# Kernel tuning notes

Measured on AMD Instinct MI355X. Metric: run time of the kernel, lower is better.

## Reference

```python
import jax, jax.numpy as jnp
import numpy as np
from jax import lax

N = 2_097_152  # grid length
WENO5_MULT_BIAS = 0.1


def _conv1d(x, w, b, pad):
    # x: [1, C_in, L], w: [C_out, C_in, K] -> [1, C_out, L]
    y = lax.conv_general_dilated(x, w, window_strides=(1,), padding=[(pad, pad)],
                                 dimension_numbers=('NCH', 'OIH', 'NCH'))
    return y + b[None, :, None]


def _inner_nn_weno5(dif, w1, b1, w2, b2, w3, b3, w4, b4, w5, b5, w6, b6):
    # dif: [N] -> multiplier signal [N] in (0,1) via sigmoid
    x = dif[None, None, :]
    x = jax.nn.elu(_conv1d(x, w1, b1, 2))
    x = jax.nn.elu(_conv1d(x, w2, b2, 2))
    x = jax.nn.elu(_conv1d(x, w3, b3, 0))
    x = jax.nn.elu(_conv1d(x, w4, b4, 0))
    x = jax.nn.elu(_conv1d(x, w5, b5, 1))
    x = jax.nn.sigmoid(_conv1d(x, w6, b6, 0))
    return x[0, 0, :]


def _avg_diff(uu):
    # centered average of forward differences, replicated at the edges -> [N]
    dif = uu[1:] - uu[:-1]
    dif_left = jnp.concatenate([dif, dif[-1:]])
    dif_right = jnp.concatenate([dif[:1], dif])
    return 0.5 * dif_left + 0.5 * dif_right


def _fluxes_minus(u):
    f0 = (11 * u[3:-2] - 7 * u[4:-1] + 2 * u[5:]) / 6
    f1 = (2 * u[2:-3] + 5 * u[3:-2] - u[4:-1]) / 6
    f2 = (-u[1:-4] + 5 * u[2:-3] + 2 * u[3:-2]) / 6
    return f0, f1, f2


def _betas_minus(u):
    b0 = 13 / 12 * (u[3:-2] - 2 * u[4:-1] + u[5:]) ** 2 + 1 / 4 * (3 * u[3:-2] - 4 * u[4:-1] + u[5:]) ** 2
    b1 = 13 / 12 * (u[2:-3] - 2 * u[3:-2] + u[4:-1]) ** 2 + 1 / 4 * (u[2:-3] - u[4:-1]) ** 2
    b2 = 13 / 12 * (u[1:-4] - 2 * u[2:-3] + u[3:-2]) ** 2 + 1 / 4 * (u[1:-4] - 4 * u[2:-3] + 3 * u[3:-2]) ** 2
    return b0, b1, b2


def _weno5(uu, e, beta_mult):
    # w5_minus=True, mweno=True, mapped=False, trainable=True branch
    ur = uu[1:]
    ul = uu[:-1]
    fp = _fluxes_minus(ur)
    fn = _fluxes_minus(ul)
    bp = _betas_minus(ur)
    bn = _betas_minus(ul)
    # multipliers bm[3+shift:-3+shift] for shift in {-1,0,1}
    mul = (beta_mult[2:-4], beta_mult[3:-3], beta_mult[4:-2])
    bp = [b * m for b, m in zip(bp, mul)]
    bn = [b * m for b, m in zip(bn, mul)]
    ds = (1 / 10, 6 / 10, 3 / 10)

    def omegas_mweno(bs):
        brs = (bs[2] - bs[0]) ** 2
        o = [d / (e + b) ** 2 * (brs + (e + b) ** 2) for b, d in zip(bs, ds)]
        s = o[0] + o[1] + o[2]
        return [x / s for x in o]

    op = omegas_mweno(bp)
    on = omegas_mweno(bn)
    fluxp = op[0] * fp[0] + op[1] * fp[1] + op[2] * fp[2]
    fluxn = on[0] * fn[0] + on[1] * fn[1] + on[2] * fn[2]
    return fluxp - fluxn  # [N-6]


def setup_inputs() -> dict:
    key = jax.random.key(0)
    ks = jax.random.split(key, 14)
    uu = jax.random.normal(ks[0], (N,), dtype=jnp.float32)
    e = jnp.float32(1e-6)
    s = 0.1  # weight scale for stability
    w1 = s * jax.random.normal(ks[1], (20, 1, 5), jnp.float32)
    b1 = s * jax.random.normal(ks[2], (20,), jnp.float32)
    w2 = s * jax.random.normal(ks[3], (40, 20, 5), jnp.float32)
    b2 = s * jax.random.normal(ks[4], (40,), jnp.float32)
    w3 = s * jax.random.normal(ks[5], (80, 40, 1), jnp.float32)
    b3 = s * jax.random.normal(ks[6], (80,), jnp.float32)
    w4 = s * jax.random.normal(ks[7], (40, 80, 1), jnp.float32)
    b4 = s * jax.random.normal(ks[8], (40,), jnp.float32)
    w5 = s * jax.random.normal(ks[9], (20, 40, 3), jnp.float32)
    b5 = s * jax.random.normal(ks[10], (20,), jnp.float32)
    w6 = s * jax.random.normal(ks[11], (1, 20, 1), jnp.float32)
    b6 = s * jax.random.normal(ks[12], (1,), jnp.float32)
    return {"uu": uu, "e": e, "w1": w1, "b1": b1, "w2": w2, "b2": b2,
            "w3": w3, "b3": b3, "w4": w4, "b4": b4, "w5": w5, "b5": b5,
            "w6": w6, "b6": b6}


def reference(uu, e, w1, b1, w2, b2, w3, b3, w4, b4, w5, b5, w6, b6):
    dif = _avg_diff(uu)
    beta_mult = _inner_nn_weno5(dif, w1, b1, w2, b2, w3, b3, w4, b4, w5, b5, w6, b6) + WENO5_MULT_BIAS
    return _weno5(uu, e, beta_mult)
```

## Files before the change

kernel.cpp:

```cpp
#include <hip/hip_runtime.h>
#include <math.h>

#define NTHREADS 512
#define TOUT 252
#define NDIF 264
#define NUU 266

#define X1S 40
#define X2S 40
#define T3AS 34
#define T3BS 50
#define X5S 26

#define SUU_OFF  0
#define SDIF_OFF 1072
#define RA_OFF   2144
#define RB_OFF   27744
#define SMEM_SIZE 48384

#define F2_BASE 0
#define F3_BASE 15
#define F4_BASE 25
#define F5_BASE 34
#define NFRAGS 42

typedef unsigned short u16;
typedef unsigned int u32;
typedef __attribute__((ext_vector_type(8))) short bf16x8;
typedef __attribute__((ext_vector_type(4))) float f32x4;

__device__ __forceinline__ float elu_f(float x) {
    return x > 0.0f ? x : (__expf(x) - 1.0f);
}
__device__ __forceinline__ float sq_f(float x) { return x * x; }
__device__ __forceinline__ u16 f2bf(float f) {
    union { float f; u32 u; } v; v.f = f;
    u32 r = v.u + 0x7FFFu + ((v.u >> 16) & 1u);
    return (u16)(r >> 16);
}
__device__ __forceinline__ float bf_lo(u32 u) {
    union { u32 u; float f; } v; v.u = u << 16; return v.f;
}
__device__ __forceinline__ float bf_hi(u32 u) {
    union { u32 u; float f; } v; v.u = u & 0xFFFF0000u; return v.f;
}
__device__ __forceinline__ u32 pack_trunc(float a, float b) {
    union { float f; u32 u; } va, vb; va.f = a; vb.f = b;
#if __has_builtin(__builtin_amdgcn_perm)
    return __builtin_amdgcn_perm(vb.u, va.u, 0x07060302u);
#else
    return (vb.u & 0xFFFF0000u) | (va.u >> 16);
#endif
}

__global__ __launch_bounds__(64) void build_frags_kernel(
    const float* __restrict__ w2, const float* __restrict__ w3,
    const float* __restrict__ w4, const float* __restrict__ w5,
    u16* __restrict__ ws)
{
    const int f = blockIdx.x;
    const int lane = threadIdx.x;
    const int m = lane & 15;
    const int q = lane >> 4;
    float wvv[8];
    #pragma unroll
    for (int j = 0; j < 8; ++j) wvv[j] = 0.0f;

    if (f < F3_BASE) {
        int mt = (f - F2_BASE) / 5, s = (f - F2_BASE) % 5;
        int oc = mt * 16 + m;
        #pragma unroll
        for (int j = 0; j < 8; ++j) {
            int ic = q * 8 + j;
            if (oc < 40 && ic < 20) wvv[j] = w2[oc * 100 + ic * 5 + s];
        }
    } else if (f < F4_BASE) {
        int mt = (f - F3_BASE) / 2, s = (f - F3_BASE) % 2;
        int oc = mt * 16 + m;
        #pragma unroll
        for (int j = 0; j < 8; ++j) {
            int k = s * 32 + q * 8 + j;
            if (k < 40) wvv[j] = w3[oc * 40 + k];
        }
    } else if (f < F5_BASE) {
        int mt = (f - F4_BASE) / 3, s = (f - F4_BASE) % 3;
        int oc = mt * 16 + m;
        #pragma unroll
        for (int j = 0; j < 8; ++j) {
            int k = s * 32 + q * 8 + j;
            if (oc < 40 && k < 80) wvv[j] = w4[oc * 80 + k];
        }
    } else {
        int mt = (f - F5_BASE) / 4, s = (f - F5_BASE) % 4;
        int oc = mt * 16 + m;
        int k0 = s * 32 + q * 8;
        int dk = k0 / 40, ic0 = k0 - dk * 40;
        #pragma unroll
        for (int j = 0; j < 8; ++j) {
            if (oc < 20 && k0 < 120) wvv[j] = w5[oc * 120 + (ic0 + j) * 3 + dk];
        }
    }
    u32 pk[4];
    #pragma unroll
    for (int p = 0; p < 4; ++p)
        pk[p] = (u32)f2bf(wvv[2 * p]) | ((u32)f2bf(wvv[2 * p + 1]) << 16);
    u32* wp = (u32*)&ws[(f * 64 + lane) * 8];
    wp[0] = pk[0]; wp[1] = pk[1]; wp[2] = pk[2]; wp[3] = pk[3];
}

__device__ __forceinline__ bf16x8 ld_frag(const u16* ws, int f, int lane) {
    return *(const bf16x8*)&ws[(f * 64 + lane) * 8];
}

__global__ __launch_bounds__(NTHREADS) void weno_nn_kernel(
    const float* __restrict__ uu, const float* __restrict__ e_ptr,
    const float* __restrict__ w1, const float* __restrict__ b1,
    const float* __restrict__ b2, const float* __restrict__ b3,
    const float* __restrict__ b4, const float* __restrict__ b5,
    const float* __restrict__ w6, const float* __restrict__ b6,
    const u16* __restrict__ wfr,
    float* __restrict__ out, int n_out, int N)
{
    __shared__ __align__(16) unsigned char smem[SMEM_SIZE];
    float* s_uu  = (float*)(smem + SUU_OFF);
    float* s_dif = (float*)(smem + SDIF_OFF);
    u16*   x1    = (u16*)(smem + RA_OFF);
    u16*   t3a   = (u16*)(smem + RA_OFF);
    u16*   t3b   = (u16*)(smem + RA_OFF);
    u16*   x5    = (u16*)(smem + RA_OFF);
    u16*   xB    = (u16*)(smem + RB_OFF);
    float* beta  = (float*)(smem + RB_OFF);

    const int tid  = threadIdx.x;
    const int lane = tid & 63;
    const int wv   = __builtin_amdgcn_readfirstlane(tid >> 6);
    const int m    = lane & 15;
    const int q    = lane >> 4;
    const int J0   = blockIdx.x * TOUT;
    const int P0   = J0 + 2;
    const int U0   = J0 - 4;

    for (int i = tid; i < NUU; i += NTHREADS) {
        int g = U0 + i;
        s_uu[i] = (g >= 0 && g < N) ? uu[g] : 0.0f;
    }
    __syncthreads();

    for (int d = tid; d < NDIF; d += NTHREADS) {
        int g = P0 - 5 + d;
        float v = 0.0f;
        if (g >= 0 && g < N) {
            int j1 = g < N - 2 ? g : N - 2;
            int j0 = g - 1 > 0 ? g - 1 : 0;
            float dl = s_uu[j1 + 1 - U0] - s_uu[j1 - U0];
            float dr = s_uu[j0 + 1 - U0] - s_uu[j0 - U0];
            v = 0.5f * (dl + dr);
        }
        s_dif[d] = v;
    }
    __syncthreads();

    if (tid < 40) ((u32*)&xB[256 * X2S])[tid] = 0;
    for (int s = tid; s < 260; s += NTHREADS) {
        int g = P0 - 3 + s;
        bool valid = (g >= 0 && g < N);
        float dv[5];
        #pragma unroll
        for (int k = 0; k < 5; ++k) dv[k] = s_dif[s + k];
        float v[20];
        #pragma unroll
        for (int oc = 0; oc < 20; ++oc) {
            float a = b1[oc];
            #pragma unroll
            for (int k = 0; k < 5; ++k) a += w1[oc * 5 + k] * dv[k];
            v[oc] = valid ? elu_f(a) : 0.0f;
        }
        u32* rp = (u32*)&x1[s * X1S];
        #pragma unroll
        for (int p = 0; p < 10; ++p)
            rp[p] = pack_trunc(v[2 * p], v[2 * p + 1]);
        #pragma unroll
        for (int p = 10; p < 16; ++p) rp[p] = 0;
    }
    __syncthreads();

    {
        bf16x8 a2[3][5];
        #pragma unroll
        for (int mt = 0; mt < 3; ++mt)
            #pragma unroll
            for (int s = 0; s < 5; ++s)
                a2[mt][s] = ld_frag(wfr, F2_BASE + mt * 5 + s, lane);
        f32x4 bias2[3];
        #pragma unroll
        for (int mt = 0; mt < 3; ++mt) {
            #pragma unroll
            for (int r = 0; r < 4; ++r) {
                int oc = mt * 16 + 4 * q + r;
                bias2[mt][r] = (oc < 40) ? b2[oc] : 0.0f;
            }
        }
        for (int t = 0; t < 2; ++t) {
            const int N0 = (wv * 2 + t) * 16;
            f32x4 acc[3];
            #pragma unroll
            for (int mt = 0; mt < 3; ++mt) acc[mt] = bias2[mt];
            #pragma unroll
            for (int s = 0; s < 5; ++s) {
                bf16x8 bfrag = *(const bf16x8*)&x1[(N0 + m + s) * X1S + q * 8];
                #pragma unroll
                for (int mt = 0; mt < 3; ++mt)
                    acc[mt] = __builtin_amdgcn_mfma_f32_16x16x32_bf16(a2[mt][s], bfrag, acc[mt], 0, 0, 0);
            }
            #pragma unroll
            for (int mt = 0; mt < 3; ++mt) {
                int oc0 = mt * 16 + 4 * q;
                if (oc0 < 40) {
                    u32* wp = (u32*)&xB[(N0 + m) * X2S + oc0];
                    wp[0] = pack_trunc(elu_f(acc[mt][0]), elu_f(acc[mt][1]));
                    wp[1] = pack_trunc(elu_f(acc[mt][2]), elu_f(acc[mt][3]));
                }
            }
        }
    }
    __syncthreads();

    bf16x8 Bx2[2][2];
    f32x4  acc4[2][3];
    #pragma unroll
    for (int t = 0; t < 2; ++t) {
        #pragma unroll
        for (int mt = 0; mt < 3; ++mt) {
            #pragma unroll
            for (int r = 0; r < 4; ++r) {
                int oc = mt * 16 + 4 * q + r;
                acc4[t][mt][r] = (oc < 40) ? b4[oc] : 0.0f;
            }
        }
    }

    for (int t = 0; t < 2; ++t) {
        const int rowi = (wv * 2 + t) * 16 + m;
        Bx2[t][0] = *(const bf16x8*)&xB[rowi * X2S + q * 8];
        Bx2[t][1] = *(const bf16x8*)&xB[rowi * X2S + ((q == 0) ? 32 : 0)];
        #pragma unroll
        for (int mt = 0; mt < 2; ++mt) {
            f32x4 a3;
            #pragma unroll
            for (int r = 0; r < 4; ++r) a3[r] = b3[mt * 16 + 4 * q + r];
            a3 = __builtin_amdgcn_mfma_f32_16x16x32_bf16(ld_frag(wfr, F3_BASE + mt * 2 + 0, lane), Bx2[t][0], a3, 0, 0, 0);
            a3 = __builtin_amdgcn_mfma_f32_16x16x32_bf16(ld_frag(wfr, F3_BASE + mt * 2 + 1, lane), Bx2[t][1], a3, 0, 0, 0);
            u32* wp = (u32*)&t3a[rowi * T3AS + mt * 16 + 4 * q];
            wp[0] = pack_trunc(elu_f(a3[0]), elu_f(a3[1]));
            wp[1] = pack_trunc(elu_f(a3[2]), elu_f(a3[3]));
        }
    }
    __syncthreads();

    for (int t = 0; t < 2; ++t) {
        const int rowi = (wv * 2 + t) * 16 + m;
        bf16x8 Bt = *(const bf16x8*)&t3a[rowi * T3AS + q * 8];
        #pragma unroll
        for (int mt = 0; mt < 3; ++mt)
            acc4[t][mt] = __builtin_amdgcn_mfma_f32_16x16x32_bf16(ld_frag(wfr, F4_BASE + mt * 3 + 0, lane), Bt, acc4[t][mt], 0, 0, 0);
    }
    __syncthreads();

    for (int t = 0; t < 2; ++t) {
        const int rowi = (wv * 2 + t) * 16 + m;
        #pragma unroll
        for (int mtb = 0; mtb < 3; ++mtb) {
            const int mt = mtb + 2;
            f32x4 a3;
            #pragma unroll
            for (int r = 0; r < 4; ++r) a3[r] = b3[mt * 16 + 4 * q + r];
            a3 = __builtin_amdgcn_mfma_f32_16x16x32_bf16(ld_frag(wfr, F3_BASE + mt * 2 + 0, lane), Bx2[t][0], a3, 0, 0, 0);
            a3 = __builtin_amdgcn_mfma_f32_16x16x32_bf16(ld_frag(wfr, F3_BASE + mt * 2 + 1, lane), Bx2[t][1], a3, 0, 0, 0);
            u32* wp = (u32*)&t3b[rowi * T3BS + mtb * 16 + 4 * q];
            wp[0] = pack_trunc(elu_f(a3[0]), elu_f(a3[1]));
            wp[1] = pack_trunc(elu_f(a3[2]), elu_f(a3[3]));
        }
    }
    __syncthreads();

    for (int t = 0; t < 2; ++t) {
        const int rowi = (wv * 2 + t) * 16 + m;
        bf16x8 Bt1 = *(const bf16x8*)&t3b[rowi * T3BS + q * 8];
        bf16x8 Bt2 = *(const bf16x8*)&t3b[rowi * T3BS + ((q < 2) ? (32 + q * 8) : 0)];
        #pragma unroll
        for (int mt = 0; mt < 3; ++mt) {
            acc4[t][mt] = __builtin_amdgcn_mfma_f32_16x16x32_bf16(ld_frag(wfr, F4_BASE + mt * 3 + 1, lane), Bt1, acc4[t][mt], 0, 0, 0);
            acc4[t][mt] = __builtin_amdgcn_mfma_f32_16x16x32_bf16(ld_frag(wfr, F4_BASE + mt * 3 + 2, lane), Bt2, acc4[t][mt], 0, 0, 0);
            int oc0 = mt * 16 + 4 * q;
            if (oc0 < 40) {
                u32* wp = (u32*)&xB[rowi * X2S + oc0];
                wp[0] = pack_trunc(elu_f(acc4[t][mt][0]), elu_f(acc4[t][mt][1]));
                wp[1] = pack_trunc(elu_f(acc4[t][mt][2]), elu_f(acc4[t][mt][3]));
            }
        }
    }
    __syncthreads();

    for (int t = 0; t < 2; ++t) {
        const int rowi = (wv * 2 + t) * 16 + m;
        bf16x8 B5[4];
        #pragma unroll
        for (int s = 0; s < 4; ++s) {
            int k0 = 32 * s + 8 * q;
            int dk, ic0;
            if (k0 < 120) {
                dk = (k0 >= 80) ? 2 : ((k0 >= 40) ? 1 : 0);
                ic0 = k0 - 40 * dk;
            } else { dk = 0; ic0 = 0; }
            B5[s] = *(const bf16x8*)&xB[(rowi + dk) * X2S + ic0];
        }
        #pragma unroll
        for (int mt = 0; mt < 2; ++mt) {
            f32x4 acc;
            #pragma unroll
            for (int r = 0; r < 4; ++r) {
                int oc = mt * 16 + 4 * q + r;
                acc[r] = (oc < 20) ? b5[oc] : 0.0f;
            }
            #pragma unroll
            for (int s = 0; s < 4; ++s)
                acc = __builtin_amdgcn_mfma_f32_16x16x32_bf16(ld_frag(wfr, F5_BASE + mt * 4 + s, lane), B5[s], acc, 0, 0, 0);
            int oc0 = mt * 16 + 4 * q;
            if (oc0 < 20) {
                u32* wp = (u32*)&x5[rowi * X5S + oc0];
                wp[0] = pack_trunc(elu_f(acc[0]), elu_f(acc[1]));
                wp[1] = pack_trunc(elu_f(acc[2]), elu_f(acc[3]));
            }
        }
    }
    __syncthreads();

    if (tid < 254) {
        const u32* xp = (const u32*)&x5[tid * X5S];
        float a = b6[0];
        #pragma unroll
        for (int p = 0; p < 10; ++p) {
            u32 u = xp[p];
            a += w6[2 * p] * bf_lo(u) + w6[2 * p + 1] * bf_hi(u);
        }
        beta[tid] = 1.0f / (1.0f + __expf(-a)) + 0.1f;
    }
    __syncthreads();

    const float eps = e_ptr[0];
    if (tid < TOUT) {
        int j = J0 + tid;
        if (j < n_out) {
            float a  = s_uu[tid + 5];
            float b  = s_uu[tid + 6];
            float c  = s_uu[tid + 7];
            float d  = s_uu[tid + 8];
            float ee = s_uu[tid + 9];
            float f  = s_uu[tid + 10];
            float m0 = beta[tid];
            float m1 = beta[tid + 1];
            float m2 = beta[tid + 2];

            const float i6 = 1.0f / 6.0f;
            float fp0 = (11.f * d - 7.f * ee + 2.f * f) * i6;
            float fp1 = (2.f * c + 5.f * d - ee) * i6;
            float fp2 = (-b + 5.f * c + 2.f * d) * i6;
            float fn0 = (11.f * c - 7.f * d + 2.f * ee) * i6;
            float fn1 = (2.f * b + 5.f * c - d) * i6;
            float fn2 = (-a + 5.f * b + 2.f * c) * i6;

            const float c1312 = 13.f / 12.f;
            float bp0 = c1312 * sq_f(d - 2.f * ee + f) + 0.25f * sq_f(3.f * d - 4.f * ee + f);
            float bp1 = c1312 * sq_f(c - 2.f * d + ee) + 0.25f * sq_f(c - ee);
            float bp2 = c1312 * sq_f(b - 2.f * c + d) + 0.25f * sq_f(b - 4.f * c + 3.f * d);
            float bn0 = c1312 * sq_f(c - 2.f * d + ee) + 0.25f * sq_f(3.f * c - 4.f * d + ee);
            float bn1 = c1312 * sq_f(b - 2.f * c + d) + 0.25f * sq_f(b - d);
            float bn2 = c1312 * sq_f(a - 2.f * b + c) + 0.25f * sq_f(a - 4.f * b + 3.f * c);

            bp0 *= m0; bp1 *= m1; bp2 *= m2;
            bn0 *= m0; bn1 *= m1; bn2 *= m2;

            float q0 = eps + bp0; q0 *= q0;
            float q1 = eps + bp1; q1 *= q1;
            float q2 = eps + bp2; q2 *= q2;
            float brs = bp2 - bp0; brs *= brs;
            float o0 = 0.1f * (1.f + brs / q0);
            float o1 = 0.6f * (1.f + brs / q1);
            float o2 = 0.3f * (1.f + brs / q2);
            float inv = 1.f / (o0 + o1 + o2);
            float fluxp = (o0 * fp0 + o1 * fp1 + o2 * fp2) * inv;

            q0 = eps + bn0; q0 *= q0;
            q1 = eps + bn1; q1 *= q1;
            q2 = eps + bn2; q2 *= q2;
            brs = bn2 - bn0; brs *= brs;
            o0 = 0.1f * (1.f + brs / q0);
            o1 = 0.6f * (1.f + brs / q1);
            o2 = 0.3f * (1.f + brs / q2);
            inv = 1.f / (o0 + o1 + o2);
            float fluxn = (o0 * fn0 + o1 * fn1 + o2 * fn2) * inv;

            out[j] = fluxp - fluxn;
        }
    }
}

extern "C" void kernel_launch(void* const* d_in, const int* in_sizes, int n_in,
                              void* d_out, int out_size, void* d_ws, size_t ws_size,
                              hipStream_t stream) {
    const float* uu = (const float*)d_in[0];
    const float* e  = (const float*)d_in[1];
    const float* w1 = (const float*)d_in[2];
    const float* b1 = (const float*)d_in[3];
    const float* w2 = (const float*)d_in[4];
    const float* b2 = (const float*)d_in[5];
    const float* w3 = (const float*)d_in[6];
    const float* b3 = (const float*)d_in[7];
    const float* w4 = (const float*)d_in[8];
    const float* b4 = (const float*)d_in[9];
    const float* w5 = (const float*)d_in[10];
    const float* b5 = (const float*)d_in[11];
    const float* w6 = (const float*)d_in[12];
    const float* b6 = (const float*)d_in[13];
    float* out = (float*)d_out;
    u16* wfr = (u16*)d_ws;
    const int N = in_sizes[0];
    const int nblocks = (out_size + TOUT - 1) / TOUT;

    build_frags_kernel<<<NFRAGS, 64, 0, stream>>>(w2, w3, w4, w5, wfr);
    weno_nn_kernel<<<nblocks, NTHREADS, 0, stream>>>(
        uu, e, w1, b1, b2, b3, b4, b5, w6, b6, wfr,
        out, out_size, N);
}
```

Before: 313.4 us.

## Halve block size and make conv3/conv4 per-wave with wave-private scratch

Shrinks the tile to 124 outputs with 256 threads and about 22KB of LDS, so more blocks fit per CU. Conv3/conv4 now run per wave, and each wave uses a private LDS scratch slice. That removes three block-wide barriers and the register-held accumulators carried across them. Conv2 weight fragments are reloaded inside the loop instead of being kept in registers. The trade-off is more halo overlap per output (extra recomputation) and more weight-fragment loads. Correctness depends on intra-wave LDS ordering with only compiler memory fences.

```diff
diff --git a/kernel.cpp b/kernel.cpp
--- a/kernel.cpp
+++ b/kernel.cpp
@@ -1,10 +1,12 @@
 #include <hip/hip_runtime.h>
 #include <math.h>
 
-#define NTHREADS 512
-#define TOUT 252
-#define NDIF 264
-#define NUU 266
+#define NTHREADS 256
+#define TOUT 124
+#define NP 128
+#define X1ROWS 132
+#define NDIF 136
+#define NUU 138
 
 #define X1S 40
 #define X2S 40
@@ -13,10 +15,10 @@
 #define X5S 26
 
 #define SUU_OFF  0
-#define SDIF_OFF 1072
-#define RA_OFF   2144
-#define RB_OFF   27744
-#define SMEM_SIZE 48384
+#define SDIF_OFF 560
+#define RA_OFF   1104
+#define RB_OFF   11664
+#define SMEM_SIZE 22080
 
 #define F2_BASE 0
 #define F3_BASE 15
@@ -28,6 +30,8 @@
 typedef unsigned int u32;
 typedef __attribute__((ext_vector_type(8))) short bf16x8;
 typedef __attribute__((ext_vector_type(4))) float f32x4;
+
+#define MEM_FENCE() __asm__ __volatile__("" ::: "memory")
 
 __device__ __forceinline__ float elu_f(float x) {
     return x > 0.0f ? x : (__expf(x) - 1.0f);
@@ -125,8 +129,7 @@
     float* s_uu  = (float*)(smem + SUU_OFF);
     float* s_dif = (float*)(smem + SDIF_OFF);
     u16*   x1    = (u16*)(smem + RA_OFF);
-    u16*   t3a   = (u16*)(smem + RA_OFF);
-    u16*   t3b   = (u16*)(smem + RA_OFF);
+    u16*   t3t   = (u16*)(smem + RA_OFF);
     u16*   x5    = (u16*)(smem + RA_OFF);
     u16*   xB    = (u16*)(smem + RB_OFF);
     float* beta  = (float*)(smem + RB_OFF);
@@ -160,8 +163,9 @@
     }
     __syncthreads();
 
-    if (tid < 40) ((u32*)&xB[256 * X2S])[tid] = 0;
-    for (int s = tid; s < 260; s += NTHREADS) {
+    if (tid >= 128 && tid < 168) ((u32*)&xB[128 * X2S])[tid - 128] = 0;
+    if (tid < X1ROWS) {
+        const int s = tid;
         int g = P0 - 3 + s;
         bool valid = (g >= 0 && g < N);
         float dv[5];
@@ -185,12 +189,6 @@
     __syncthreads();
 
     {
-        bf16x8 a2[3][5];
-        #pragma unroll
-        for (int mt = 0; mt < 3; ++mt)
-            #pragma unroll
-            for (int s = 0; s < 5; ++s)
-                a2[mt][s] = ld_frag(wfr, F2_BASE + mt * 5 + s, lane);
         f32x4 bias2[3];
         #pragma unroll
         for (int mt = 0; mt < 3; ++mt) {
@@ -201,22 +199,23 @@
             }
         }
         for (int t = 0; t < 2; ++t) {
-            const int N0 = (wv * 2 + t) * 16;
+            const int rowi = (wv * 2 + t) * 16 + m;
             f32x4 acc[3];
             #pragma unroll
             for (int mt = 0; mt < 3; ++mt) acc[mt] = bias2[mt];
             #pragma unroll
             for (int s = 0; s < 5; ++s) {
-                bf16x8 bfrag = *(const bf16x8*)&x1[(N0 + m + s) * X1S + q * 8];
+                bf16x8 bfrag = *(const bf16x8*)&x1[(rowi + s) * X1S + q * 8];
                 #pragma unroll
                 for (int mt = 0; mt < 3; ++mt)
-                    acc[mt] = __builtin_amdgcn_mfma_f32_16x16x32_bf16(a2[mt][s], bfrag, acc[mt], 0, 0, 0);
+                    acc[mt] = __builtin_amdgcn_mfma_f32_16x16x32_bf16(
+                        ld_frag(wfr, F2_BASE + mt * 5 + s, lane), bfrag, acc[mt], 0, 0, 0);
             }
             #pragma unroll
             for (int mt = 0; mt < 3; ++mt) {
                 int oc0 = mt * 16 + 4 * q;
                 if (oc0 < 40) {
-                    u32* wp = (u32*)&xB[(N0 + m) * X2S + oc0];
+                    u32* wp = (u32*)&xB[rowi * X2S + oc0];
                     wp[0] = pack_trunc(elu_f(acc[mt][0]), elu_f(acc[mt][1]));
                     wp[1] = pack_trunc(elu_f(acc[mt][2]), elu_f(acc[mt][3]));
                 }
@@ -225,78 +224,70 @@
     }
     __syncthreads();
 
-    bf16x8 Bx2[2][2];
-    f32x4  acc4[2][3];
-    #pragma unroll
-    for (int t = 0; t < 2; ++t) {
-        #pragma unroll
-        for (int mt = 0; mt < 3; ++mt) {
-            #pragma unroll
-            for (int r = 0; r < 4; ++r) {
-                int oc = mt * 16 + 4 * q + r;
-                acc4[t][mt][r] = (oc < 40) ? b4[oc] : 0.0f;
-            }
-        }
-    }
-
-    for (int t = 0; t < 2; ++t) {
-        const int rowi = (wv * 2 + t) * 16 + m;
-        Bx2[t][0] = *(const bf16x8*)&xB[rowi * X2S + q * 8];
-        Bx2[t][1] = *(const bf16x8*)&xB[rowi * X2S + ((q == 0) ? 32 : 0)];
-        #pragma unroll
-        for (int mt = 0; mt < 2; ++mt) {
-            f32x4 a3;
-            #pragma unroll
-            for (int r = 0; r < 4; ++r) a3[r] = b3[mt * 16 + 4 * q + r];
-            a3 = __builtin_amdgcn_mfma_f32_16x16x32_bf16(ld_frag(wfr, F3_BASE + mt * 2 + 0, lane), Bx2[t][0], a3, 0, 0, 0);
-            a3 = __builtin_amdgcn_mfma_f32_16x16x32_bf16(ld_frag(wfr, F3_BASE + mt * 2 + 1, lane), Bx2[t][1], a3, 0, 0, 0);
-            u32* wp = (u32*)&t3a[rowi * T3AS + mt * 16 + 4 * q];
-            wp[0] = pack_trunc(elu_f(a3[0]), elu_f(a3[1]));
-            wp[1] = pack_trunc(elu_f(a3[2]), elu_f(a3[3]));
-        }
-    }
-    __syncthreads();
-
-    for (int t = 0; t < 2; ++t) {
-        const int rowi = (wv * 2 + t) * 16 + m;
-        bf16x8 Bt = *(const bf16x8*)&t3a[rowi * T3AS + q * 8];
-        #pragma unroll
-        for (int mt = 0; mt < 3; ++mt)
-            acc4[t][mt] = __builtin_amdgcn_mfma_f32_16x16x32_bf16(ld_frag(wfr, F4_BASE + mt * 3 + 0, lane), Bt, acc4[t][mt], 0, 0, 0);
-    }
-    __syncthreads();
-
-    for (int t = 0; t < 2; ++t) {
-        const int rowi = (wv * 2 + t) * 16 + m;
-        #pragma unroll
-        for (int mtb = 0; mtb < 3; ++mtb) {
-            const int mt = mtb + 2;
-            f32x4 a3;
-            #pragma unroll
-            for (int r = 0; r < 4; ++r) a3[r] = b3[mt * 16 + 4 * q + r];
-            a3 = __builtin_amdgcn_mfma_f32_16x16x32_bf16(ld_frag(wfr, F3_BASE + mt * 2 + 0, lane), Bx2[t][0], a3, 0, 0, 0);
-            a3 = __builtin_amdgcn_mfma_f32_16x16x32_bf16(ld_frag(wfr, F3_BASE + mt * 2 + 1, lane), Bx2[t][1], a3, 0, 0, 0);
-            u32* wp = (u32*)&t3b[rowi * T3BS + mtb * 16 + 4 * q];
-            wp[0] = pack_trunc(elu_f(a3[0]), elu_f(a3[1]));
-            wp[1] = pack_trunc(elu_f(a3[2]), elu_f(a3[3]));
-        }
-    }
-    __syncthreads();
-
-    for (int t = 0; t < 2; ++t) {
-        const int rowi = (wv * 2 + t) * 16 + m;
-        bf16x8 Bt1 = *(const bf16x8*)&t3b[rowi * T3BS + q * 8];
-        bf16x8 Bt2 = *(const bf16x8*)&t3b[rowi * T3BS + ((q < 2) ? (32 + q * 8) : 0)];
-        #pragma unroll
-        for (int mt = 0; mt < 3; ++mt) {
-            acc4[t][mt] = __builtin_amdgcn_mfma_f32_16x16x32_bf16(ld_frag(wfr, F4_BASE + mt * 3 + 1, lane), Bt1, acc4[t][mt], 0, 0, 0);
-            acc4[t][mt] = __builtin_amdgcn_mfma_f32_16x16x32_bf16(ld_frag(wfr, F4_BASE + mt * 3 + 2, lane), Bt2, acc4[t][mt], 0, 0, 0);
-            int oc0 = mt * 16 + 4 * q;
-            if (oc0 < 40) {
-                u32* wp = (u32*)&xB[rowi * X2S + oc0];
-                wp[0] = pack_trunc(elu_f(acc4[t][mt][0]), elu_f(acc4[t][mt][1]));
-                wp[1] = pack_trunc(elu_f(acc4[t][mt][2]), elu_f(acc4[t][mt][3]));
-            }
+    {
+        u16* t3w = t3t + wv * (16 * T3BS);
+        for (int t = 0; t < 2; ++t) {
+            const int rowi = (wv * 2 + t) * 16 + m;
+            bf16x8 Bx2_0 = *(const bf16x8*)&xB[rowi * X2S + q * 8];
+            bf16x8 Bx2_1 = *(const bf16x8*)&xB[rowi * X2S + ((q == 0) ? 32 : 0)];
+
+            #pragma unroll
+            for (int mt = 0; mt < 2; ++mt) {
+                f32x4 a3;
+                #pragma unroll
+                for (int r = 0; r < 4; ++r) a3[r] = b3[mt * 16 + 4 * q + r];
+                a3 = __builtin_amdgcn_mfma_f32_16x16x32_bf16(ld_frag(wfr, F3_BASE + mt * 2 + 0, lane), Bx2_0, a3, 0, 0, 0);
+                a3 = __builtin_amdgcn_mfma_f32_16x16x32_bf16(ld_frag(wfr, F3_BASE + mt * 2 + 1, lane), Bx2_1, a3, 0, 0, 0);
+                u32* wp = (u32*)&t3w[m * T3AS + mt * 16 + 4 * q];
+                wp[0] = pack_trunc(elu_f(a3[0]), elu_f(a3[1]));
+                wp[1] = pack_trunc(elu_f(a3[2]), elu_f(a3[3]));
+            }
+            MEM_FENCE();
+            f32x4 acc4[3];
+            #pragma unroll
+            for (int mt = 0; mt < 3; ++mt) {
+                #pragma unroll
+                for (int r = 0; r < 4; ++r) {
+                    int oc = mt * 16 + 4 * q + r;
+                    acc4[mt][r] = (oc < 40) ? b4[oc] : 0.0f;
+                }
+            }
+            {
+                bf16x8 Bt = *(const bf16x8*)&t3w[m * T3AS + q * 8];
+                #pragma unroll
+                for (int mt = 0; mt < 3; ++mt)
+                    acc4[mt] = __builtin_amdgcn_mfma_f32_16x16x32_bf16(ld_frag(wfr, F4_BASE + mt * 3 + 0, lane), Bt, acc4[mt], 0, 0, 0);
+            }
+            MEM_FENCE();
+            #pragma unroll
+            for (int mtb = 0; mtb < 3; ++mtb) {
+                const int mt = mtb + 2;
+                f32x4 a3;
+                #pragma unroll
+                for (int r = 0; r < 4; ++r) a3[r] = b3[mt * 16 + 4 * q + r];
+                a3 = __builtin_amdgcn_mfma_f32_16x16x32_bf16(ld_frag(wfr, F3_BASE + mt * 2 + 0, lane), Bx2_0, a3, 0, 0, 0);
+                a3 = __builtin_amdgcn_mfma_f32_16x16x32_bf16(ld_frag(wfr, F3_BASE + mt * 2 + 1, lane), Bx2_1, a3, 0, 0, 0);
+                u32* wp = (u32*)&t3w[m * T3BS + mtb * 16 + 4 * q];
+                wp[0] = pack_trunc(elu_f(a3[0]), elu_f(a3[1]));
+                wp[1] = pack_trunc(elu_f(a3[2]), elu_f(a3[3]));
+            }
+            MEM_FENCE();
+            {
+                bf16x8 Bt1 = *(const bf16x8*)&t3w[m * T3BS + q * 8];
+                bf16x8 Bt2 = *(const bf16x8*)&t3w[m * T3BS + ((q < 2) ? (32 + q * 8) : 0)];
+                #pragma unroll
+                for (int mt = 0; mt < 3; ++mt) {
+                    acc4[mt] = __builtin_amdgcn_mfma_f32_16x16x32_bf16(ld_frag(wfr, F4_BASE + mt * 3 + 1, lane), Bt1, acc4[mt], 0, 0, 0);
+                    acc4[mt] = __builtin_amdgcn_mfma_f32_16x16x32_bf16(ld_frag(wfr, F4_BASE + mt * 3 + 2, lane), Bt2, acc4[mt], 0, 0, 0);
+                    int oc0 = mt * 16 + 4 * q;
+                    if (oc0 < 40) {
+                        u32* wp = (u32*)&xB[rowi * X2S + oc0];
+                        wp[0] = pack_trunc(elu_f(acc4[mt][0]), elu_f(acc4[mt][1]));
+                        wp[1] = pack_trunc(elu_f(acc4[mt][2]), elu_f(acc4[mt][3]));
+                    }
+                }
+            }
+            MEM_FENCE();
         }
     }
     __syncthreads();
@@ -335,7 +326,7 @@
     }
     __syncthreads();
 
-    if (tid < 254) {
+    if (tid < TOUT + 2) {
         const u32* xp = (const u32*)&x5[tid * X5S];
         float a = b6[0];
         #pragma unroll
```

Result: no change. 310.0 us (-1.1%).
